# Performance work log

Hardware: AMD Instinct MI355X
Metric: run time of the kernel (lower is better)

Reference implementation:

```python
import jax, jax.numpy as jnp
import numpy as np

DIM = 128
H = 8
HD = DIM // H
NL = 6
DFF = 2048
EPS = 1e-5
S2S_STEPS = 6


def _ln(x, g, b):
    m = jnp.mean(x, -1, keepdims=True)
    v = jnp.mean(jnp.square(x - m), -1, keepdims=True)
    return (x - m) / jnp.sqrt(v + EPS) * g + b


def _lstm_step(x, h, c, wih, whh, bih, bhh):
    # torch LSTM gate order: i, f, g, o
    gates = x @ wih.T + bih + h @ whh.T + bhh
    i, f, g, o = jnp.split(gates, 4, axis=-1)
    c = jax.nn.sigmoid(f) * c + jax.nn.sigmoid(i) * jnp.tanh(g)
    h = jax.nn.sigmoid(o) * jnp.tanh(c)
    return h, c


def setup_inputs() -> dict:
    key = jax.random.key(0)
    ks = iter(jax.random.split(key, 16))
    n = lambda shape: jax.random.normal(next(ks), shape, jnp.float32) * 0.02
    inp = {
        "data": jax.random.normal(next(ks), (64, 256, 3), jnp.float32),
        "lin0_w": n((DIM, 3)), "lin0_b": jnp.zeros((DIM,), jnp.float32),
        "attn_in_w": n((NL, 3 * DIM, DIM)), "attn_in_b": jnp.zeros((NL, 3 * DIM), jnp.float32),
        "attn_out_w": n((NL, DIM, DIM)), "attn_out_b": jnp.zeros((NL, DIM), jnp.float32),
        "ln1_g": jnp.ones((NL, DIM), jnp.float32), "ln1_b": jnp.zeros((NL, DIM), jnp.float32),
        "ff_w1": n((NL, DFF, DIM)), "ff_b1": jnp.zeros((NL, DFF), jnp.float32),
        "ff_w2": n((NL, DIM, DFF)), "ff_b2": jnp.zeros((NL, DIM), jnp.float32),
        "ln2_g": jnp.ones((NL, DIM), jnp.float32), "ln2_b": jnp.zeros((NL, DIM), jnp.float32),
        "s2s_wih": n((4 * DIM, 2 * DIM)), "s2s_whh": n((4 * DIM, DIM)),
        "s2s_bih": jnp.zeros((4 * DIM,), jnp.float32), "s2s_bhh": jnp.zeros((4 * DIM,), jnp.float32),
        "mem_wih": n((4 * DIM, 2 * DIM)), "mem_whh": n((4 * DIM, DIM)),
        "mem_bih": jnp.zeros((4 * DIM,), jnp.float32), "mem_bhh": jnp.zeros((4 * DIM,), jnp.float32),
        "lin1_w": n((DIM, DIM)), "lin1_b": jnp.zeros((DIM,), jnp.float32),
        "lin3_w": n((1, DIM)), "lin3_b": jnp.zeros((1,), jnp.float32),
    }
    return inp


def reference(data, lin0_w, lin0_b, attn_in_w, attn_in_b, attn_out_w, attn_out_b,
              ln1_g, ln1_b, ff_w1, ff_b1, ff_w2, ff_b2, ln2_g, ln2_b,
              s2s_wih, s2s_whh, s2s_bih, s2s_bhh,
              mem_wih, mem_whh, mem_bih, mem_bhh,
              lin1_w, lin1_b, lin3_w, lin3_b):
    x = jax.nn.relu(data @ lin0_w.T + lin0_b)  # [S=64, B=256, D]
    S, B, _ = x.shape
    # torch TransformerEncoder with batch_first=False: attention over axis 0,
    # axis 1 is the transformer batch. Post-norm layers (norm_first=False), relu FFN.
    for l in range(NL):
        qkv = x @ attn_in_w[l].T + attn_in_b[l]
        q, k, v = jnp.split(qkv, 3, axis=-1)
        q = q.reshape(S, B, H, HD)
        k = k.reshape(S, B, H, HD)
        v = v.reshape(S, B, H, HD)
        scores = jnp.einsum('sbhd,tbhd->bhst', q, k) / np.float32(np.sqrt(HD))
        attn = jax.nn.softmax(scores, axis=-1)
        ao = jnp.einsum('bhst,tbhd->sbhd', attn, v).reshape(S, B, DIM)
        x = _ln(x + ao @ attn_out_w[l].T + attn_out_b[l], ln1_g[l], ln1_b[l])
        ff = jax.nn.relu(x @ ff_w1[l].T + ff_b1[l]) @ ff_w2[l].T + ff_b2[l]
        x = _ln(x + ff, ln2_g[l], ln2_b[l])
    # Set2Set pooling: bidxs assign segment = axis-0 index for each block of
    # num_atoms consecutive rows of flatten(out,0,1), i.e. pool over axis 1.
    q_star = jnp.zeros((S, 2 * DIM), x.dtype)
    h = jnp.zeros((S, DIM), x.dtype)
    c = jnp.zeros((S, DIM), x.dtype)
    for _ in range(S2S_STEPS):
        h, c = _lstm_step(q_star, h, c, s2s_wih, s2s_whh, s2s_bih, s2s_bhh)
        e = jnp.einsum('bnd,bd->bn', x, h)          # [S, num_atoms]
        a = jax.nn.softmax(e, axis=-1)              # segment softmax (uniform segs)
        r = jnp.einsum('bn,bnd->bd', a, x)          # segment weighted sum
        q_star = jnp.concatenate([h, r], axis=-1)   # [S, 2D]
    # memory LSTM: seq_len 1, zero initial state (states=None branch)
    hx = jnp.zeros((S, DIM), x.dtype)
    cx = jnp.zeros((S, DIM), x.dtype)
    hx, cx = _lstm_step(q_star, hx, cx, mem_wih, mem_whh, mem_bih, mem_bhh)
    o = jax.nn.relu(hx @ lin1_w.T + lin1_b)
    v_out = (o @ lin3_w.T + lin3_b)[None]  # [1, S, 1]
    return v_out, hx[None], cx[None]
```

## Files before the change

kernel.cpp:

```cpp
#include <hip/hip_runtime.h>
#include <math.h>


typedef _Float16 __attribute__((ext_vector_type(8))) f16x8;
typedef __attribute__((ext_vector_type(4))) float f32x4;
typedef _Float16 __attribute__((ext_vector_type(2))) h16x2;

__device__ __forceinline__ unsigned short f2h(float f) {
  union { _Float16 h; unsigned short s; } x; x.h = (_Float16)f; return x.s;
}
__device__ __forceinline__ float h2f(unsigned short u) {
  union { unsigned short s; _Float16 h; } x; x.s = u; return (float)x.h;
}
__device__ __forceinline__ unsigned packh(float a, float b) {
  return (unsigned)f2h(a) | ((unsigned)f2h(b) << 16);
}
__device__ __forceinline__ float hlo(unsigned u) {
  union { unsigned short s; _Float16 h; } x; x.s = (unsigned short)(u & 0xffff);
  return (float)x.h;
}
__device__ __forceinline__ float hhi(unsigned u) {
  union { unsigned short s; _Float16 h; } x; x.s = (unsigned short)(u >> 16);
  return (float)x.h;
}
__device__ __forceinline__ float fdot2u(unsigned a, unsigned b, float c) {
#if __has_builtin(__builtin_amdgcn_fdot2)
  union U { unsigned u; h16x2 h; };
  U x, y; x.u = a; y.u = b;
  return __builtin_amdgcn_fdot2(x.h, y.h, c, false);
#else
  return c + hlo(a) * hlo(b) + hhi(a) * hhi(b);
#endif
}
__device__ __forceinline__ float sigf(float x) { return 1.f / (1.f + expf(-x)); }

__device__ __forceinline__ void gl2lds16(const void* g, void* l) {
  __builtin_amdgcn_global_load_lds(
      (const __attribute__((address_space(1))) unsigned int*)g,
      (__attribute__((address_space(3))) unsigned int*)l, 16, 0, 0);
}

__global__ __launch_bounds__(256) void convw_kernel(
    const float* __restrict__ aiw, const float* __restrict__ aow,
    const float* __restrict__ w1, const float* __restrict__ w2,
    const float* __restrict__ wih, const float* __restrict__ whh,
    const float* __restrict__ mwih,
    unsigned short* __restrict__ o0, unsigned short* __restrict__ o1,
    unsigned short* __restrict__ o2, unsigned short* __restrict__ o3,
    unsigned short* __restrict__ o4, unsigned short* __restrict__ o5,
    unsigned short* __restrict__ o6) {
  int i = blockIdx.x * 256 + threadIdx.x;
  if (i < 294912) {
    int l = i / 49152, o = i % 49152;
    int j = o & 7, fr = (o >> 3) & 15, fq = (o >> 7) & 3, ks = (o >> 9) & 3,
        rb = o >> 11;
    o0[i] = f2h(aiw[l * 49152 + (rb * 16 + fr) * 128 + ks * 32 + fq * 8 + j]);
  } else if (i < 393216) {
    int ii = i - 294912;
    int l = ii / 16384, o = ii % 16384;
    int j = o & 7, fr = (o >> 3) & 15, fq = (o >> 7) & 3, ks = (o >> 9) & 3,
        rb = o >> 11;
    o1[ii] = f2h(aow[l * 16384 + (rb * 16 + fr) * 128 + ks * 32 + fq * 8 + j]);
  } else if (i < 1966080) {
    int ii = i - 393216;
    int l = ii >> 18, o = ii & 262143;
    int j = o & 7, fr = (o >> 3) & 15, fq = (o >> 7) & 3, ks = (o >> 9) & 3,
        rb = o >> 11;
    o2[ii] = f2h(w1[l * 262144 + (rb * 16 + fr) * 128 + ks * 32 + fq * 8 + j]);
  } else if (i < 3538944) {
    int ii = i - 1966080;
    int l = ii >> 18, o = ii & 262143;
    int j = o & 7, fr = (o >> 3) & 15, fq = (o >> 7) & 3, ks = (o >> 9) & 63,
        rb = o >> 15;
    o3[ii] = f2h(w2[l * 262144 + (rb * 16 + fr) * 2048 + ks * 32 + fq * 8 + j]);
  } else if (i < 3670016) {
    int j = i - 3538944; o4[j] = f2h(wih[j]);
  } else if (i < 3735552) {
    int j = i - 3670016; o5[j] = f2h(whh[j]);
  } else {
    int j = i - 3735552; o6[j] = f2h(mwih[j]);
  }
}

__global__ __launch_bounds__(256) void lin0_kernel(
    const float* __restrict__ data, const float* __restrict__ w,
    const float* __restrict__ b, float* __restrict__ x,
    unsigned short* __restrict__ xb) {
  int i = blockIdx.x * 256 + threadIdx.x;
  int n = i >> 7, d = i & 127;
  float v = b[d] + data[n * 3 + 0] * w[d * 3 + 0]
                 + data[n * 3 + 1] * w[d * 3 + 1]
                 + data[n * 3 + 2] * w[d * 3 + 2];
  v = fmaxf(v, 0.0f);
  x[i] = v;
  xb[i] = f2h(v);
}

__global__ __launch_bounds__(512) void layer_kernel(
    const unsigned short* __restrict__ xbg,
    const unsigned short* __restrict__ wqkv, const float* __restrict__ bqkv,
    const unsigned short* __restrict__ wout, const float* __restrict__ bout,
    const float* __restrict__ ln1g, const float* __restrict__ ln1b,
    const unsigned short* __restrict__ w1, const float* __restrict__ b1,
    const unsigned short* __restrict__ w2, const float* __restrict__ b2,
    const float* __restrict__ ln2g, const float* __restrict__ ln2b,
    float* __restrict__ xio, unsigned short* __restrict__ xbo) {
  __shared__ __align__(16) unsigned short Xs[64 * 128];
  __shared__ __align__(16) unsigned short Ws[256 * 128];
  __shared__ __align__(16) unsigned short U1[128 * 128];
  __shared__ __align__(16) unsigned short U2[128 * 128];
  __shared__ __align__(16) uint4 zchunk;
  __shared__ float psum[8][64], psq[8][64];
  __shared__ float2 stats[64];

  unsigned short* Qs = U1;
  unsigned short* Ks2 = U1 + 8192;
  unsigned short* VT = U2;
  unsigned short* AOs = U2 + 8192;

  int tid = threadIdx.x, w = tid >> 6, lane = tid & 63;
  int b = blockIdx.x;
  int r4 = lane >> 4, cs = lane & 15;
  int fr = lane & 15, fq = lane >> 4;

  if (tid == 0) zchunk = make_uint4(0u, 0u, 0u, 0u);

#pragma unroll
  for (int i = 0; i < 2; i++) {
    int issue = w * 2 + i;
    int row = issue * 4 + r4;
    int g = cs ^ (row & 7);
    gl2lds16(xbg + (size_t)(row * 256 + b) * 128 + g * 8,
             (char*)Xs + issue * 1024);
  }
  f16x8 bqk[4][2];
#pragma unroll
  for (int ks = 0; ks < 4; ks++)
#pragma unroll
    for (int ni = 0; ni < 2; ni++)
      bqk[ks][ni] = *(const f16x8*)(wqkv + (w * 2 + ni) * 2048 + ks * 512 +
                                    fq * 128 + fr * 8);
  __syncthreads();

  f16x8 xfragA[4][4];
#pragma unroll
  for (int ks = 0; ks < 4; ks++)
#pragma unroll
    for (int mi = 0; mi < 4; mi++) {
      int row = mi * 16 + fr;
      int kq = (ks * 4 + fq) ^ (row & 7);
      xfragA[ks][mi] = *(const f16x8*)(Xs + row * 128 + kq * 8);
    }

  {
    f32x4 acc[4][2];
#pragma unroll
    for (int i = 0; i < 4; i++)
#pragma unroll
      for (int j = 0; j < 2; j++) acc[i][j] = (f32x4){0.f, 0.f, 0.f, 0.f};
#pragma unroll
    for (int ks = 0; ks < 4; ks++)
#pragma unroll
      for (int mi = 0; mi < 4; mi++)
#pragma unroll
        for (int ni = 0; ni < 2; ni++)
          acc[mi][ni] = __builtin_amdgcn_mfma_f32_16x16x32_f16(
              xfragA[ks][mi], bqk[ks][ni], acc[mi][ni], 0, 0, 0);
#pragma unroll
    for (int ni = 0; ni < 2; ni++) {
      int c = (w * 2 + ni) * 16 + fr;
      float bv = bqkv[c];
      unsigned short* dst = (c < 128) ? Qs : Ks2;
      int cc = c & 127;
#pragma unroll
      for (int mi = 0; mi < 4; mi++)
#pragma unroll
        for (int r = 0; r < 4; r++) {
          int row = mi * 16 + fq * 4 + r;
          dst[row * 128 + (((cc >> 3) ^ (row & 7)) << 3) + (cc & 7)] =
              f2h(acc[mi][ni][r] + bv);
        }
    }
  }
  f16x8 bv4[4];
#pragma unroll
  for (int ks = 0; ks < 4; ks++)
    bv4[ks] = *(const f16x8*)(wqkv + (16 + w) * 2048 + ks * 512 + fq * 128 +
                              fr * 8);
  __syncthreads();

  {
    f32x4 acc[4];
#pragma unroll
    for (int i = 0; i < 4; i++) acc[i] = (f32x4){0.f, 0.f, 0.f, 0.f};
#pragma unroll
    for (int ks = 0; ks < 4; ks++)
#pragma unroll
      for (int mi = 0; mi < 4; mi++)
        acc[mi] = __builtin_amdgcn_mfma_f32_16x16x32_f16(xfragA[ks][mi],
                                                         bv4[ks], acc[mi],
                                                         0, 0, 0);
    int f = w * 16 + fr;
    float bv = bqkv[256 + f];
#pragma unroll
    for (int mi = 0; mi < 4; mi++)
#pragma unroll
      for (int r = 0; r < 4; r++) {
        int srow = mi * 16 + fq * 4 + r;
        VT[f * 64 + (((srow >> 3) ^ (f & 7)) << 3) + (srow & 7)] =
            f2h(acc[mi][r] + bv);
      }
  }
  __syncthreads();

  {
    int h = w;
    unsigned short* Pb = Ws + w * 4096;
    f32x4 sc[4][4];
#pragma unroll
    for (int i = 0; i < 4; i++)
#pragma unroll
      for (int j = 0; j < 4; j++) sc[i][j] = (f32x4){0.f, 0.f, 0.f, 0.f};
    {
      f16x8 af[4], bf[4];
#pragma unroll
      for (int mi = 0; mi < 4; mi++) {
        int row = mi * 16 + fr;
        const unsigned short* pa =
            (fq < 2) ? (Qs + row * 128 + (((h * 2 + fq) ^ (row & 7)) << 3))
                     : (const unsigned short*)&zchunk;
        af[mi] = *(const f16x8*)pa;
      }
#pragma unroll
      for (int ti = 0; ti < 4; ti++) {
        int trow = ti * 16 + fr;
        const unsigned short* pb =
            (fq < 2) ? (Ks2 + trow * 128 + (((h * 2 + fq) ^ (trow & 7)) << 3))
                     : (const unsigned short*)&zchunk;
        bf[ti] = *(const f16x8*)pb;
      }
#pragma unroll
      for (int mi = 0; mi < 4; mi++)
#pragma unroll
        for (int ti = 0; ti < 4; ti++)
          sc[mi][ti] = __builtin_amdgcn_mfma_f32_16x16x32_f16(
              af[mi], bf[ti], sc[mi][ti], 0, 0, 0);
    }
#pragma unroll
    for (int mi = 0; mi < 4; mi++) {
#pragma unroll
      for (int r = 0; r < 4; r++) {
        float m = -1e30f;
#pragma unroll
        for (int ti = 0; ti < 4; ti++) m = fmaxf(m, sc[mi][ti][r]);
        m = fmaxf(m, __shfl_xor(m, 1, 64));
        m = fmaxf(m, __shfl_xor(m, 2, 64));
        m = fmaxf(m, __shfl_xor(m, 4, 64));
        m = fmaxf(m, __shfl_xor(m, 8, 64));
        m *= 0.25f;
        float ss = 0.f;
#pragma unroll
        for (int ti = 0; ti < 4; ti++) {
          float p = expf(sc[mi][ti][r] * 0.25f - m);
          sc[mi][ti][r] = p;
          ss += p;
        }
        ss += __shfl_xor(ss, 1, 64);
        ss += __shfl_xor(ss, 2, 64);
        ss += __shfl_xor(ss, 4, 64);
        ss += __shfl_xor(ss, 8, 64);
        float inv = 1.f / ss;
        int prow = mi * 16 + fq * 4 + r;
#pragma unroll
        for (int ti = 0; ti < 4; ti++) {
          int t = ti * 16 + fr;
          Pb[prow * 64 + (((t >> 3) ^ (prow & 7)) << 3) + (t & 7)] =
              f2h(sc[mi][ti][r] * inv);
        }
      }
    }
    f32x4 po[4];
#pragma unroll
    for (int i = 0; i < 4; i++) po[i] = (f32x4){0.f, 0.f, 0.f, 0.f};
#pragma unroll
    for (int ks2 = 0; ks2 < 2; ks2++) {
      f16x8 af[4], bf;
#pragma unroll
      for (int si = 0; si < 4; si++) {
        int prow = si * 16 + fr;
        int kq = (ks2 * 4 + fq) ^ (prow & 7);
        af[si] = *(const f16x8*)(Pb + prow * 64 + kq * 8);
      }
      {
        int vrow = h * 16 + fr;
        int kq = (ks2 * 4 + fq) ^ (vrow & 7);
        bf = *(const f16x8*)(VT + vrow * 64 + kq * 8);
      }
#pragma unroll
      for (int si = 0; si < 4; si++)
        po[si] = __builtin_amdgcn_mfma_f32_16x16x32_f16(af[si], bf, po[si],
                                                        0, 0, 0);
    }
#pragma unroll
    for (int si = 0; si < 4; si++)
#pragma unroll
      for (int r = 0; r < 4; r++) {
        int arow = si * 16 + fq * 4 + r;
        int c = h * 16 + fr;
        AOs[arow * 128 + (((c >> 3) ^ (arow & 7)) << 3) + (c & 7)] =
            f2h(po[si][r]);
      }
  }
  f16x8 bwo[4];
#pragma unroll
  for (int ks = 0; ks < 4; ks++)
    bwo[ks] = *(const f16x8*)(wout + w * 2048 + ks * 512 + fq * 128 + fr * 8);
  __syncthreads();

  {
    f32x4 acc[4];
#pragma unroll
    for (int i = 0; i < 4; i++) acc[i] = (f32x4){0.f, 0.f, 0.f, 0.f};
#pragma unroll
    for (int ks = 0; ks < 4; ks++) {
      f16x8 af[4];
#pragma unroll
      for (int si = 0; si < 4; si++) {
        int row = si * 16 + fr;
        int kq = (ks * 4 + fq) ^ (row & 7);
        af[si] = *(const f16x8*)(AOs + row * 128 + kq * 8);
      }
#pragma unroll
      for (int si = 0; si < 4; si++)
        acc[si] = __builtin_amdgcn_mfma_f32_16x16x32_f16(af[si], bwo[ks],
                                                         acc[si], 0, 0, 0);
    }
    int c = w * 16 + fr;
    float bv = bout[c];
    float vv4[4][4];
    float sums[4][4], sqs[4][4];
#pragma unroll
    for (int si = 0; si < 4; si++)
#pragma unroll
      for (int r = 0; r < 4; r++) {
        int row = si * 16 + fq * 4 + r;
        float v = acc[si][r] + bv + xio[(size_t)(row * 256 + b) * 128 + c];
        vv4[si][r] = v;
        sums[si][r] = v;
        sqs[si][r] = v * v;
      }
#pragma unroll
    for (int d = 1; d < 16; d <<= 1) {
#pragma unroll
      for (int si = 0; si < 4; si++)
#pragma unroll
        for (int r = 0; r < 4; r++) {
          sums[si][r] += __shfl_xor(sums[si][r], d, 64);
          sqs[si][r] += __shfl_xor(sqs[si][r], d, 64);
        }
    }
    if (fr == 0) {
#pragma unroll
      for (int si = 0; si < 4; si++)
#pragma unroll
        for (int r = 0; r < 4; r++) {
          int row = si * 16 + fq * 4 + r;
          psum[w][row] = sums[si][r];
          psq[w][row] = sqs[si][r];
        }
    }
    __syncthreads();
    if (tid < 64) {
      float S = 0.f, Q = 0.f;
#pragma unroll
      for (int ww = 0; ww < 8; ww++) { S += psum[ww][tid]; Q += psq[ww][tid]; }
      float m = S * (1.f / 128.f);
      float var = Q * (1.f / 128.f) - m * m;
      stats[tid] = make_float2(m, rsqrtf(var + 1e-5f));
    }
    __syncthreads();
    float gl = ln1g[c], bl = ln1b[c];
#pragma unroll
    for (int si = 0; si < 4; si++)
#pragma unroll
      for (int r = 0; r < 4; r++) {
        int row = si * 16 + fq * 4 + r;
        float2 st2 = stats[row];
        float y = (vv4[si][r] - st2.x) * st2.y * gl + bl;
        Xs[row * 128 + (((c >> 3) ^ (row & 7)) << 3) + (c & 7)] = f2h(y);
      }
  }
  __syncthreads();

  f16x8 xfragF[4][4];
#pragma unroll
  for (int ks = 0; ks < 4; ks++)
#pragma unroll
    for (int mi = 0; mi < 4; mi++) {
      int row = mi * 16 + fr;
      int kq = (ks * 4 + fq) ^ (row & 7);
      xfragF[ks][mi] = *(const f16x8*)(Xs + row * 128 + kq * 8);
    }

  f32x4 acc2[4];
#pragma unroll
  for (int i = 0; i < 4; i++) acc2[i] = (f32x4){0.f, 0.f, 0.f, 0.f};

  for (int c = 0; c < 16; c++) {
    unsigned short* Hcur = Ws + (c & 1) * 8192;
    f16x8 bw1[4], bw2[4];
#pragma unroll
    for (int ks = 0; ks < 4; ks++)
      bw1[ks] = *(const f16x8*)(w1 + (size_t)(c * 8 + w) * 2048 + ks * 512 +
                                fq * 128 + fr * 8);
#pragma unroll
    for (int ks = 0; ks < 4; ks++)
      bw2[ks] = *(const f16x8*)(w2 + (size_t)w * 32768 + (c * 4 + ks) * 512 +
                                fq * 128 + fr * 8);
    f32x4 acc1[4];
#pragma unroll
    for (int i = 0; i < 4; i++) acc1[i] = (f32x4){0.f, 0.f, 0.f, 0.f};
#pragma unroll
    for (int ks = 0; ks < 4; ks++)
#pragma unroll
      for (int mi = 0; mi < 4; mi++)
        acc1[mi] = __builtin_amdgcn_mfma_f32_16x16x32_f16(xfragF[ks][mi],
                                                          bw1[ks], acc1[mi],
                                                          0, 0, 0);
    {
      int col = w * 16 + fr;
      float bv = b1[c * 128 + col];
#pragma unroll
      for (int mi = 0; mi < 4; mi++)
#pragma unroll
        for (int r = 0; r < 4; r++) {
          int row = mi * 16 + fq * 4 + r;
          Hcur[row * 128 + (((col >> 3) ^ (row & 7)) << 3) + (col & 7)] =
              f2h(fmaxf(acc1[mi][r] + bv, 0.f));
        }
    }
    __syncthreads();
#pragma unroll
    for (int ks = 0; ks < 4; ks++) {
      f16x8 af[4];
#pragma unroll
      for (int si = 0; si < 4; si++) {
        int row = si * 16 + fr;
        int kq = (ks * 4 + fq) ^ (row & 7);
        af[si] = *(const f16x8*)(Hcur + row * 128 + kq * 8);
      }
#pragma unroll
      for (int si = 0; si < 4; si++)
        acc2[si] = __builtin_amdgcn_mfma_f32_16x16x32_f16(af[si], bw2[ks],
                                                          acc2[si], 0, 0, 0);
    }
  }

  {
    int c = w * 16 + fr;
    float bv = b2[c];
    float vv4[4][4];
    float sums[4][4], sqs[4][4];
#pragma unroll
    for (int si = 0; si < 4; si++)
#pragma unroll
      for (int r = 0; r < 4; r++) {
        int row = si * 16 + fq * 4 + r;
        float resid =
            h2f(Xs[row * 128 + (((c >> 3) ^ (row & 7)) << 3) + (c & 7)]);
        float v = acc2[si][r] + bv + resid;
        vv4[si][r] = v;
        sums[si][r] = v;
        sqs[si][r] = v * v;
      }
#pragma unroll
    for (int d = 1; d < 16; d <<= 1) {
#pragma unroll
      for (int si = 0; si < 4; si++)
#pragma unroll
        for (int r = 0; r < 4; r++) {
          sums[si][r] += __shfl_xor(sums[si][r], d, 64);
          sqs[si][r] += __shfl_xor(sqs[si][r], d, 64);
        }
    }
    if (fr == 0) {
#pragma unroll
      for (int si = 0; si < 4; si++)
#pragma unroll
        for (int r = 0; r < 4; r++) {
          int row = si * 16 + fq * 4 + r;
          psum[w][row] = sums[si][r];
          psq[w][row] = sqs[si][r];
        }
    }
    __syncthreads();
    if (tid < 64) {
      float S = 0.f, Q = 0.f;
#pragma unroll
      for (int ww = 0; ww < 8; ww++) { S += psum[ww][tid]; Q += psq[ww][tid]; }
      float m = S * (1.f / 128.f);
      float var = Q * (1.f / 128.f) - m * m;
      stats[tid] = make_float2(m, rsqrtf(var + 1e-5f));
    }
    __syncthreads();
    float gl = ln2g[c], bl = ln2b[c];
#pragma unroll
    for (int si = 0; si < 4; si++)
#pragma unroll
      for (int r = 0; r < 4; r++) {
        int row = si * 16 + fq * 4 + r;
        float2 st = stats[row];
        float y = (vv4[si][r] - st.x) * st.y * gl + bl;
        size_t o = (size_t)(row * 256 + b) * 128 + c;
        xio[o] = y;
        xbo[o] = f2h(y);
      }
  }
}

__global__ __launch_bounds__(512, 1) void s2s_kernel(
    const unsigned short* __restrict__ xb,
    const unsigned short* __restrict__ wihh,
    const unsigned short* __restrict__ whhh,
    const float* __restrict__ bih, const float* __restrict__ bhh,
    const unsigned short* __restrict__ mwihh,
    const float* __restrict__ mbih, const float* __restrict__ mbhh,
    const float* __restrict__ l1w, const float* __restrict__ l1b,
    const float* __restrict__ l3w, const float* __restrict__ l3b,
    float* __restrict__ out) {
  __shared__ __align__(16) unsigned xl[256 * 65];
  __shared__ __align__(16) unsigned qu[128];
  __shared__ __align__(16) float cst[128];
  __shared__ __align__(16) float gates[512];
  __shared__ __align__(16) float red[256];
  __shared__ __align__(16) float aw[256];
  int s = blockIdx.x, t = threadIdx.x, lane = t & 63, w = t >> 6;

  uint4 wreg[32], ureg[16];
  {
    const uint4* wp = (const uint4*)(wihh + (size_t)t * 256);
#pragma unroll
    for (int i = 0; i < 32; i++) wreg[i] = wp[i];
    const uint4* up = (const uint4*)(whhh + (size_t)t * 128);
#pragma unroll
    for (int i = 0; i < 16; i++) ureg[i] = up[i];
  }

  const uint4* xs4 = (const uint4*)(xb + (size_t)s * 32768);
#pragma unroll
  for (int it = 0; it < 8; it++) {
    int f = it * 512 + t;
    uint4 v = xs4[f];
    int n = f >> 4, jc = (f & 15) * 4;
    unsigned* dst = xl + n * 65 + jc;
    dst[0] = v.x; dst[1] = v.y; dst[2] = v.z; dst[3] = v.w;
  }
  if (t < 128) cst[t] = 0.f;
  __syncthreads();

  const uint4* q4 = (const uint4*)qu;
  float bsum = bih[t] + bhh[t];

  for (int step = 0; step < 6; step++) {
    if (step > 0) {
      float a0 = 0.f, a1 = 0.f, a2 = 0.f, a3 = 0.f;
#pragma unroll
      for (int i = 0; i < 16; i++) {
        uint4 qv = q4[i];
        a0 = fdot2u(wreg[i].x, qv.x, a0);
        a1 = fdot2u(wreg[i].y, qv.y, a1);
        a2 = fdot2u(wreg[i].z, qv.z, a2);
        a3 = fdot2u(wreg[i].w, qv.w, a3);
        a0 = fdot2u(ureg[i].x, qv.x, a0);
        a1 = fdot2u(ureg[i].y, qv.y, a1);
        a2 = fdot2u(ureg[i].z, qv.z, a2);
        a3 = fdot2u(ureg[i].w, qv.w, a3);
      }
#pragma unroll
      for (int i = 16; i < 32; i++) {
        uint4 qv = q4[i];
        a0 = fdot2u(wreg[i].x, qv.x, a0);
        a1 = fdot2u(wreg[i].y, qv.y, a1);
        a2 = fdot2u(wreg[i].z, qv.z, a2);
        a3 = fdot2u(wreg[i].w, qv.w, a3);
      }
      gates[t] = bsum + ((a0 + a1) + (a2 + a3));
    } else {
      gates[t] = bsum;
    }
    __syncthreads();
    if (t < 128) {
      float ig = sigf(gates[t]), fg = sigf(gates[128 + t]);
      float gg = tanhf(gates[256 + t]), og = sigf(gates[384 + t]);
      float cn = fg * cst[t] + ig * gg;
      cst[t] = cn;
      float hn = og * tanhf(cn);
      float hp = __shfl_xor(hn, 1, 64);
      if ((t & 1) == 0) qu[t >> 1] = packh(hn, hp);
    }
    __syncthreads();
    if (step > 0) {
      int n = t >> 1, p = t & 1;
      const unsigned* xr = xl + n * 65 + p * 32;
      float e0 = 0.f, e1 = 0.f;
#pragma unroll 8
      for (int i = 0; i < 32; i += 2) {
        e0 = fdot2u(xr[i], qu[p * 32 + i], e0);
        e1 = fdot2u(xr[i + 1], qu[p * 32 + i + 1], e1);
      }
      float e = e0 + e1;
      e += __shfl_xor(e, 1, 64);
      if (p == 0) red[n] = e;
      __syncthreads();
      float v0 = red[lane], v1 = red[64 + lane];
      float v2 = red[128 + lane], v3 = red[192 + lane];
      float m = fmaxf(fmaxf(v0, v1), fmaxf(v2, v3));
#pragma unroll
      for (int d = 1; d < 64; d <<= 1) m = fmaxf(m, __shfl_xor(m, d, 64));
      float p0 = expf(v0 - m), p1 = expf(v1 - m);
      float p2 = expf(v2 - m), p3 = expf(v3 - m);
      float ss = p0 + p1 + p2 + p3;
#pragma unroll
      for (int d = 1; d < 64; d <<= 1) ss += __shfl_xor(ss, d, 64);
      float Sinv = 1.f / ss;
      if (w == 0) {
        aw[lane] = p0 * Sinv; aw[64 + lane] = p1 * Sinv;
        aw[128 + lane] = p2 * Sinv; aw[192 + lane] = p3 * Sinv;
      }
    } else {
      if (t < 256) aw[t] = 1.f / 256.f;
    }
    __syncthreads();
    {
      int d = t & 127, grp = t >> 7;
      const unsigned* xc = xl + grp * 64 * 65 + (d >> 1);
      int hi = d & 1;
      const float* ap = aw + grp * 64;
      float r = 0.f;
#pragma unroll 8
      for (int n2 = 0; n2 < 64; n2++) {
        unsigned u = xc[n2 * 65];
        r += ap[n2] * (hi ? hhi(u) : hlo(u));
      }
      gates[t] = r;
    }
    __syncthreads();
    if (t < 128) {
      float rd = gates[t] + gates[128 + t] + gates[256 + t] + gates[384 + t];
      float rp = __shfl_xor(rd, 1, 64);
      if ((t & 1) == 0) qu[64 + (t >> 1)] = packh(rd, rp);
    }
    __syncthreads();
  }
  {
    float a0 = 0.f, a1 = 0.f, a2 = 0.f, a3 = 0.f;
    const uint4* mp = (const uint4*)(mwihh + (size_t)t * 256);
#pragma unroll 8
    for (int i = 0; i < 32; i++) {
      uint4 wv = mp[i], qv = q4[i];
      a0 = fdot2u(wv.x, qv.x, a0);
      a1 = fdot2u(wv.y, qv.y, a1);
      a2 = fdot2u(wv.z, qv.z, a2);
      a3 = fdot2u(wv.w, qv.w, a3);
    }
    gates[t] = mbih[t] + mbhh[t] + ((a0 + a1) + (a2 + a3));
  }
  __syncthreads();
  if (t < 128) {
    float ig = sigf(gates[t]);
    float gg = tanhf(gates[256 + t]);
    float og = sigf(gates[384 + t]);
    float cx = ig * gg;
    float hx = og * tanhf(cx);
    cst[t] = hx;
    out[64 + s * 128 + t] = hx;
    out[64 + 8192 + s * 128 + t] = cx;
  }
  __syncthreads();
  if (t < 128) {
    float acc = l1b[t];
    const float4* w4 = (const float4*)(l1w + (size_t)t * 128);
    const float4* h4 = (const float4*)cst;
#pragma unroll 8
    for (int k = 0; k < 32; k++) {
      float4 a = w4[k], b = h4[k];
      acc += a.x * b.x + a.y * b.y + a.z * b.z + a.w * b.w;
    }
    red[t] = fmaxf(acc, 0.f) * l3w[t];
  } else if (t < 256) {
    red[t] = 0.f;
  }
  __syncthreads();
  for (int off = 128; off; off >>= 1) {
    if (t < off) red[t] += red[t + off];
    __syncthreads();
  }
  if (t == 0) out[s] = red[0] + l3b[0];
}

extern "C" void kernel_launch(void* const* d_in, const int* in_sizes, int n_in,
                              void* d_out, int out_size, void* d_ws,
                              size_t ws_size, hipStream_t stream) {
  const float* data       = (const float*)d_in[0];
  const float* lin0_w     = (const float*)d_in[1];
  const float* lin0_b     = (const float*)d_in[2];
  const float* attn_in_w  = (const float*)d_in[3];
  const float* attn_in_b  = (const float*)d_in[4];
  const float* attn_out_w = (const float*)d_in[5];
  const float* attn_out_b = (const float*)d_in[6];
  const float* ln1_g      = (const float*)d_in[7];
  const float* ln1_b      = (const float*)d_in[8];
  const float* ff_w1      = (const float*)d_in[9];
  const float* ff_b1      = (const float*)d_in[10];
  const float* ff_w2      = (const float*)d_in[11];
  const float* ff_b2      = (const float*)d_in[12];
  const float* ln2_g      = (const float*)d_in[13];
  const float* ln2_b      = (const float*)d_in[14];
  const float* s2s_wih    = (const float*)d_in[15];
  const float* s2s_whh    = (const float*)d_in[16];
  const float* s2s_bih    = (const float*)d_in[17];
  const float* s2s_bhh    = (const float*)d_in[18];
  const float* mem_wih    = (const float*)d_in[19];
  const float* mem_bih    = (const float*)d_in[21];
  const float* mem_bhh    = (const float*)d_in[22];
  const float* lin1_w     = (const float*)d_in[23];
  const float* lin1_b     = (const float*)d_in[24];
  const float* lin3_w     = (const float*)d_in[25];
  const float* lin3_b     = (const float*)d_in[26];
  float* out = (float*)d_out;

  char* p = (char*)d_ws;
  float* x = (float*)p;                      p += (size_t)16384 * 128 * 4;
  unsigned short* xb = (unsigned short*)p;   p += (size_t)16384 * 128 * 2;
  unsigned short* wqkv = (unsigned short*)p; p += (size_t)294912 * 2;
  unsigned short* wout = (unsigned short*)p; p += (size_t)98304 * 2;
  unsigned short* w1h = (unsigned short*)p;  p += (size_t)1572864 * 2;
  unsigned short* w2h = (unsigned short*)p;  p += (size_t)1572864 * 2;
  unsigned short* wihh = (unsigned short*)p; p += (size_t)131072 * 2;
  unsigned short* whhh = (unsigned short*)p; p += (size_t)65536 * 2;
  unsigned short* mwihh = (unsigned short*)p; p += (size_t)131072 * 2;

  convw_kernel<<<15104, 256, 0, stream>>>(
      attn_in_w, attn_out_w, ff_w1, ff_w2, s2s_wih, s2s_whh, mem_wih,
      wqkv, wout, w1h, w2h, wihh, whhh, mwihh);
  lin0_kernel<<<8192, 256, 0, stream>>>(data, lin0_w, lin0_b, x, xb);

  for (int l = 0; l < 6; l++) {
    layer_kernel<<<256, 512, 0, stream>>>(
        xb, wqkv + (size_t)l * 49152, attn_in_b + l * 384,
        wout + (size_t)l * 16384, attn_out_b + l * 128,
        ln1_g + l * 128, ln1_b + l * 128,
        w1h + (size_t)l * 262144, ff_b1 + l * 2048,
        w2h + (size_t)l * 262144, ff_b2 + l * 128,
        ln2_g + l * 128, ln2_b + l * 128, x, xb);
  }

  s2s_kernel<<<64, 512, 0, stream>>>(
      xb, wihh, whhh, s2s_bih, s2s_bhh,
      mwihh, mem_bih, mem_bhh, lin1_w, lin1_b, lin3_w, lin3_b, out);
}
```

Measured before the change: 459.4 us.

## Split layer kernel into two blocks per batch column with half-row ownership

The fused transformer layer kernel now launches 512 blocks of 256 threads instead of 256 blocks of 512. Each block still computes full Q/K/V for all 64 sequence rows, but handles attention output, the out-projection, LayerNorms and the FFN for only its half (32 rows). Shared memory is trimmed by reusing buffers (Q/K region for P and FFN hidden, Xs for attention output), which lets two blocks fit per CU. This doubles the grid on a 256-CU device to improve occupancy and latency hiding, at the cost of duplicating the QKV projection in both blocks and reloading weight fragments inside loops instead of keeping them in registers.

```diff
diff --git a/kernel.cpp b/kernel.cpp
--- a/kernel.cpp
+++ b/kernel.cpp
@@ -96,7 +96,7 @@
   xb[i] = f2h(v);
 }
 
-__global__ __launch_bounds__(512) void layer_kernel(
+__global__ __launch_bounds__(256, 2) void layer_kernel(
     const unsigned short* __restrict__ xbg,
     const unsigned short* __restrict__ wqkv, const float* __restrict__ bqkv,
     const unsigned short* __restrict__ wout, const float* __restrict__ bout,
@@ -106,40 +106,30 @@
     const float* __restrict__ ln2g, const float* __restrict__ ln2b,
     float* __restrict__ xio, unsigned short* __restrict__ xbo) {
   __shared__ __align__(16) unsigned short Xs[64 * 128];
-  __shared__ __align__(16) unsigned short Ws[256 * 128];
-  __shared__ __align__(16) unsigned short U1[128 * 128];
-  __shared__ __align__(16) unsigned short U2[128 * 128];
+  __shared__ __align__(16) unsigned short QKP[16384];
+  __shared__ __align__(16) unsigned short VT[128 * 64];
   __shared__ __align__(16) uint4 zchunk;
-  __shared__ float psum[8][64], psq[8][64];
-  __shared__ float2 stats[64];
-
-  unsigned short* Qs = U1;
-  unsigned short* Ks2 = U1 + 8192;
-  unsigned short* VT = U2;
-  unsigned short* AOs = U2 + 8192;
+  __shared__ float psum[4][32], psq[4][32];
+  __shared__ float2 stats[32];
+
+  unsigned short* Qs = QKP;
+  unsigned short* Ks2 = QKP + 8192;
 
   int tid = threadIdx.x, w = tid >> 6, lane = tid & 63;
-  int b = blockIdx.x;
+  int b = blockIdx.x >> 1, half = blockIdx.x & 1;
   int r4 = lane >> 4, cs = lane & 15;
   int fr = lane & 15, fq = lane >> 4;
 
   if (tid == 0) zchunk = make_uint4(0u, 0u, 0u, 0u);
 
 #pragma unroll
-  for (int i = 0; i < 2; i++) {
-    int issue = w * 2 + i;
+  for (int i = 0; i < 4; i++) {
+    int issue = w * 4 + i;
     int row = issue * 4 + r4;
     int g = cs ^ (row & 7);
     gl2lds16(xbg + (size_t)(row * 256 + b) * 128 + g * 8,
              (char*)Xs + issue * 1024);
   }
-  f16x8 bqk[4][2];
-#pragma unroll
-  for (int ks = 0; ks < 4; ks++)
-#pragma unroll
-    for (int ni = 0; ni < 2; ni++)
-      bqk[ks][ni] = *(const f16x8*)(wqkv + (w * 2 + ni) * 2048 + ks * 512 +
-                                    fq * 128 + fr * 8);
   __syncthreads();
 
   f16x8 xfragA[4][4];
@@ -153,22 +143,28 @@
     }
 
   {
-    f32x4 acc[4][2];
+    f32x4 acc[4][4];
 #pragma unroll
     for (int i = 0; i < 4; i++)
 #pragma unroll
-      for (int j = 0; j < 2; j++) acc[i][j] = (f32x4){0.f, 0.f, 0.f, 0.f};
-#pragma unroll
-    for (int ks = 0; ks < 4; ks++)
+      for (int j = 0; j < 4; j++) acc[i][j] = (f32x4){0.f, 0.f, 0.f, 0.f};
+#pragma unroll
+    for (int ks = 0; ks < 4; ks++) {
+      f16x8 bf[4];
+#pragma unroll
+      for (int ni = 0; ni < 4; ni++)
+        bf[ni] = *(const f16x8*)(wqkv + (w * 4 + ni) * 2048 + ks * 512 +
+                                 fq * 128 + fr * 8);
 #pragma unroll
       for (int mi = 0; mi < 4; mi++)
 #pragma unroll
-        for (int ni = 0; ni < 2; ni++)
+        for (int ni = 0; ni < 4; ni++)
           acc[mi][ni] = __builtin_amdgcn_mfma_f32_16x16x32_f16(
-              xfragA[ks][mi], bqk[ks][ni], acc[mi][ni], 0, 0, 0);
-#pragma unroll
-    for (int ni = 0; ni < 2; ni++) {
-      int c = (w * 2 + ni) * 16 + fr;
+              xfragA[ks][mi], bf[ni], acc[mi][ni], 0, 0, 0);
+    }
+#pragma unroll
+    for (int ni = 0; ni < 4; ni++) {
+      int c = (w * 4 + ni) * 16 + fr;
       float bv = bqkv[c];
       unsigned short* dst = (c < 128) ? Qs : Ks2;
       int cc = c & 127;
@@ -182,54 +178,56 @@
         }
     }
   }
-  f16x8 bv4[4];
-#pragma unroll
-  for (int ks = 0; ks < 4; ks++)
-    bv4[ks] = *(const f16x8*)(wqkv + (16 + w) * 2048 + ks * 512 + fq * 128 +
-                              fr * 8);
   __syncthreads();
 
   {
-    f32x4 acc[4];
-#pragma unroll
-    for (int i = 0; i < 4; i++) acc[i] = (f32x4){0.f, 0.f, 0.f, 0.f};
-#pragma unroll
-    for (int ks = 0; ks < 4; ks++)
+    f32x4 acc[2][4];
+#pragma unroll
+    for (int i = 0; i < 2; i++)
+#pragma unroll
+      for (int j = 0; j < 4; j++) acc[i][j] = (f32x4){0.f, 0.f, 0.f, 0.f};
+#pragma unroll
+    for (int ks = 0; ks < 4; ks++) {
+      f16x8 bf[2];
+#pragma unroll
+      for (int fi = 0; fi < 2; fi++)
+        bf[fi] = *(const f16x8*)(wqkv + (16 + w * 2 + fi) * 2048 + ks * 512 +
+                                 fq * 128 + fr * 8);
+#pragma unroll
+      for (int fi = 0; fi < 2; fi++)
+#pragma unroll
+        for (int mi = 0; mi < 4; mi++)
+          acc[fi][mi] = __builtin_amdgcn_mfma_f32_16x16x32_f16(
+              xfragA[ks][mi], bf[fi], acc[fi][mi], 0, 0, 0);
+    }
+#pragma unroll
+    for (int fi = 0; fi < 2; fi++) {
+      int f = (w * 2 + fi) * 16 + fr;
+      float bv = bqkv[256 + f];
 #pragma unroll
       for (int mi = 0; mi < 4; mi++)
-        acc[mi] = __builtin_amdgcn_mfma_f32_16x16x32_f16(xfragA[ks][mi],
-                                                         bv4[ks], acc[mi],
-                                                         0, 0, 0);
-    int f = w * 16 + fr;
-    float bv = bqkv[256 + f];
-#pragma unroll
-    for (int mi = 0; mi < 4; mi++)
-#pragma unroll
-      for (int r = 0; r < 4; r++) {
-        int srow = mi * 16 + fq * 4 + r;
-        VT[f * 64 + (((srow >> 3) ^ (f & 7)) << 3) + (srow & 7)] =
-            f2h(acc[mi][r] + bv);
-      }
+#pragma unroll
+        for (int r = 0; r < 4; r++) {
+          int srow = mi * 16 + fq * 4 + r;
+          VT[f * 64 + (((srow >> 3) ^ (f & 7)) << 3) + (srow & 7)] =
+              f2h(acc[fi][mi][r] + bv);
+        }
+    }
   }
   __syncthreads();
 
   {
-    int h = w;
-    unsigned short* Pb = Ws + w * 4096;
-    f32x4 sc[4][4];
-#pragma unroll
-    for (int i = 0; i < 4; i++)
-#pragma unroll
-      for (int j = 0; j < 4; j++) sc[i][j] = (f32x4){0.f, 0.f, 0.f, 0.f};
-    {
-      f16x8 af[4], bf[4];
-#pragma unroll
-      for (int mi = 0; mi < 4; mi++) {
-        int row = mi * 16 + fr;
+    f16x8 afH[2][2], bfH[2][4];
+#pragma unroll
+    for (int hi = 0; hi < 2; hi++) {
+      int h = w * 2 + hi;
+#pragma unroll
+      for (int mi2 = 0; mi2 < 2; mi2++) {
+        int rowg = half * 32 + mi2 * 16 + fr;
         const unsigned short* pa =
-            (fq < 2) ? (Qs + row * 128 + (((h * 2 + fq) ^ (row & 7)) << 3))
+            (fq < 2) ? (Qs + rowg * 128 + (((h * 2 + fq) ^ (rowg & 7)) << 3))
                      : (const unsigned short*)&zchunk;
-        af[mi] = *(const f16x8*)pa;
+        afH[hi][mi2] = *(const f16x8*)pa;
       }
 #pragma unroll
       for (int ti = 0; ti < 4; ti++) {
@@ -237,284 +235,332 @@
         const unsigned short* pb =
             (fq < 2) ? (Ks2 + trow * 128 + (((h * 2 + fq) ^ (trow & 7)) << 3))
                      : (const unsigned short*)&zchunk;
-        bf[ti] = *(const f16x8*)pb;
-      }
-#pragma unroll
-      for (int mi = 0; mi < 4; mi++)
+        bfH[hi][ti] = *(const f16x8*)pb;
+      }
+    }
+    __syncthreads();
+
+#pragma unroll
+    for (int hi = 0; hi < 2; hi++) {
+      int h = w * 2 + hi;
+      unsigned short* Pb = QKP + (w * 2 + hi) * 2048;
+      f32x4 sc[2][4];
+#pragma unroll
+      for (int i = 0; i < 2; i++)
+#pragma unroll
+        for (int j = 0; j < 4; j++) sc[i][j] = (f32x4){0.f, 0.f, 0.f, 0.f};
+#pragma unroll
+      for (int mi2 = 0; mi2 < 2; mi2++)
 #pragma unroll
         for (int ti = 0; ti < 4; ti++)
-          sc[mi][ti] = __builtin_amdgcn_mfma_f32_16x16x32_f16(
-              af[mi], bf[ti], sc[mi][ti], 0, 0, 0);
-    }
-#pragma unroll
-    for (int mi = 0; mi < 4; mi++) {
-#pragma unroll
-      for (int r = 0; r < 4; r++) {
-        float m = -1e30f;
-#pragma unroll
-        for (int ti = 0; ti < 4; ti++) m = fmaxf(m, sc[mi][ti][r]);
-        m = fmaxf(m, __shfl_xor(m, 1, 64));
-        m = fmaxf(m, __shfl_xor(m, 2, 64));
-        m = fmaxf(m, __shfl_xor(m, 4, 64));
-        m = fmaxf(m, __shfl_xor(m, 8, 64));
-        m *= 0.25f;
-        float ss = 0.f;
-#pragma unroll
-        for (int ti = 0; ti < 4; ti++) {
-          float p = expf(sc[mi][ti][r] * 0.25f - m);
-          sc[mi][ti][r] = p;
-          ss += p;
-        }
-        ss += __shfl_xor(ss, 1, 64);
-        ss += __shfl_xor(ss, 2, 64);
-        ss += __shfl_xor(ss, 4, 64);
-        ss += __shfl_xor(ss, 8, 64);
-        float inv = 1.f / ss;
-        int prow = mi * 16 + fq * 4 + r;
-#pragma unroll
-        for (int ti = 0; ti < 4; ti++) {
-          int t = ti * 16 + fr;
-          Pb[prow * 64 + (((t >> 3) ^ (prow & 7)) << 3) + (t & 7)] =
-              f2h(sc[mi][ti][r] * inv);
-        }
-      }
-    }
-    f32x4 po[4];
-#pragma unroll
-    for (int i = 0; i < 4; i++) po[i] = (f32x4){0.f, 0.f, 0.f, 0.f};
-#pragma unroll
-    for (int ks2 = 0; ks2 < 2; ks2++) {
-      f16x8 af[4], bf;
-#pragma unroll
-      for (int si = 0; si < 4; si++) {
-        int prow = si * 16 + fr;
-        int kq = (ks2 * 4 + fq) ^ (prow & 7);
-        af[si] = *(const f16x8*)(Pb + prow * 64 + kq * 8);
-      }
-      {
-        int vrow = h * 16 + fr;
-        int kq = (ks2 * 4 + fq) ^ (vrow & 7);
-        bf = *(const f16x8*)(VT + vrow * 64 + kq * 8);
-      }
-#pragma unroll
-      for (int si = 0; si < 4; si++)
-        po[si] = __builtin_amdgcn_mfma_f32_16x16x32_f16(af[si], bf, po[si],
-                                                        0, 0, 0);
-    }
-#pragma unroll
-    for (int si = 0; si < 4; si++)
-#pragma unroll
-      for (int r = 0; r < 4; r++) {
-        int arow = si * 16 + fq * 4 + r;
-        int c = h * 16 + fr;
-        AOs[arow * 128 + (((c >> 3) ^ (arow & 7)) << 3) + (c & 7)] =
-            f2h(po[si][r]);
-      }
-  }
-  f16x8 bwo[4];
-#pragma unroll
-  for (int ks = 0; ks < 4; ks++)
-    bwo[ks] = *(const f16x8*)(wout + w * 2048 + ks * 512 + fq * 128 + fr * 8);
+          sc[mi2][ti] = __builtin_amdgcn_mfma_f32_16x16x32_f16(
+              afH[hi][mi2], bfH[hi][ti], sc[mi2][ti], 0, 0, 0);
+#pragma unroll
+      for (int mi2 = 0; mi2 < 2; mi2++) {
+#pragma unroll
+        for (int r = 0; r < 4; r++) {
+          float m = -1e30f;
+#pragma unroll
+          for (int ti = 0; ti < 4; ti++) m = fmaxf(m, sc[mi2][ti][r]);
+          m = fmaxf(m, __shfl_xor(m, 1, 64));
+          m = fmaxf(m, __shfl_xor(m, 2, 64));
+          m = fmaxf(m, __shfl_xor(m, 4, 64));
+          m = fmaxf(m, __shfl_xor(m, 8, 64));
+          m *= 0.25f;
+          float ss = 0.f;
+#pragma unroll
+          for (int ti = 0; ti < 4; ti++) {
+            float p = expf(sc[mi2][ti][r] * 0.25f - m);
+            sc[mi2][ti][r] = p;
+            ss += p;
+          }
+          ss += __shfl_xor(ss, 1, 64);
+          ss += __shfl_xor(ss, 2, 64);
+          ss += __shfl_xor(ss, 4, 64);
+          ss += __shfl_xor(ss, 8, 64);
+          float inv = 1.f / ss;
+          int prow = mi2 * 16 + fq * 4 + r;
+#pragma unroll
+          for (int ti = 0; ti < 4; ti++) {
+            int t = ti * 16 + fr;
+            Pb[prow * 64 + (((t >> 3) ^ (prow & 7)) << 3) + (t & 7)] =
+                f2h(sc[mi2][ti][r] * inv);
+          }
+        }
+      }
+      f32x4 po[2];
+#pragma unroll
+      for (int i = 0; i < 2; i++) po[i] = (f32x4){0.f, 0.f, 0.f, 0.f};
+#pragma unroll
+      for (int ks2 = 0; ks2 < 2; ks2++) {
+        f16x8 af[2], bf;
+#pragma unroll
+        for (int si2 = 0; si2 < 2; si2++) {
+          int prow = si2 * 16 + fr;
+          int kq = (ks2 * 4 + fq) ^ (prow & 7);
+          af[si2] = *(const f16x8*)(Pb + prow * 64 + kq * 8);
+        }
+        {
+          int vrow = h * 16 + fr;
+          int kq = (ks2 * 4 + fq) ^ (vrow & 7);
+          bf = *(const f16x8*)(VT + vrow * 64 + kq * 8);
+        }
+#pragma unroll
+        for (int si2 = 0; si2 < 2; si2++)
+          po[si2] = __builtin_amdgcn_mfma_f32_16x16x32_f16(af[si2], bf,
+                                                           po[si2], 0, 0, 0);
+      }
+#pragma unroll
+      for (int si2 = 0; si2 < 2; si2++)
+#pragma unroll
+        for (int r = 0; r < 4; r++) {
+          int arow = si2 * 16 + fq * 4 + r;
+          int c = h * 16 + fr;
+          Xs[arow * 128 + (((c >> 3) ^ (arow & 7)) << 3) + (c & 7)] =
+              f2h(po[si2][r]);
+        }
+    }
+  }
   __syncthreads();
 
+  float vv4[2][2][4];
   {
-    f32x4 acc[4];
-#pragma unroll
-    for (int i = 0; i < 4; i++) acc[i] = (f32x4){0.f, 0.f, 0.f, 0.f};
+    f32x4 acc[2][2];
+#pragma unroll
+    for (int i = 0; i < 2; i++)
+#pragma unroll
+      for (int j = 0; j < 2; j++) acc[i][j] = (f32x4){0.f, 0.f, 0.f, 0.f};
 #pragma unroll
     for (int ks = 0; ks < 4; ks++) {
-      f16x8 af[4];
-#pragma unroll
-      for (int si = 0; si < 4; si++) {
-        int row = si * 16 + fr;
-        int kq = (ks * 4 + fq) ^ (row & 7);
-        af[si] = *(const f16x8*)(AOs + row * 128 + kq * 8);
-      }
-#pragma unroll
-      for (int si = 0; si < 4; si++)
-        acc[si] = __builtin_amdgcn_mfma_f32_16x16x32_f16(af[si], bwo[ks],
-                                                         acc[si], 0, 0, 0);
-    }
-    int c = w * 16 + fr;
-    float bv = bout[c];
-    float vv4[4][4];
-    float sums[4][4], sqs[4][4];
-#pragma unroll
-    for (int si = 0; si < 4; si++)
-#pragma unroll
-      for (int r = 0; r < 4; r++) {
-        int row = si * 16 + fq * 4 + r;
-        float v = acc[si][r] + bv + xio[(size_t)(row * 256 + b) * 128 + c];
-        vv4[si][r] = v;
-        sums[si][r] = v;
-        sqs[si][r] = v * v;
-      }
+      f16x8 af[2], bwo[2];
+#pragma unroll
+      for (int si2 = 0; si2 < 2; si2++) {
+        int rowl = si2 * 16 + fr;
+        int kq = (ks * 4 + fq) ^ (rowl & 7);
+        af[si2] = *(const f16x8*)(Xs + rowl * 128 + kq * 8);
+      }
+#pragma unroll
+      for (int ni = 0; ni < 2; ni++)
+        bwo[ni] = *(const f16x8*)(wout + (w * 2 + ni) * 2048 + ks * 512 +
+                                  fq * 128 + fr * 8);
+#pragma unroll
+      for (int si2 = 0; si2 < 2; si2++)
+#pragma unroll
+        for (int ni = 0; ni < 2; ni++)
+          acc[si2][ni] = __builtin_amdgcn_mfma_f32_16x16x32_f16(
+              af[si2], bwo[ni], acc[si2][ni], 0, 0, 0);
+    }
+    float sums[2][4], sqs[2][4];
+#pragma unroll
+    for (int si2 = 0; si2 < 2; si2++)
+#pragma unroll
+      for (int r = 0; r < 4; r++) { sums[si2][r] = 0.f; sqs[si2][r] = 0.f; }
+#pragma unroll
+    for (int ni = 0; ni < 2; ni++) {
+      int c = (w * 2 + ni) * 16 + fr;
+      float bv = bout[c];
+#pragma unroll
+      for (int si2 = 0; si2 < 2; si2++)
+#pragma unroll
+        for (int r = 0; r < 4; r++) {
+          int rowl = si2 * 16 + fq * 4 + r;
+          int rowg = half * 32 + rowl;
+          float v = acc[si2][ni][r] + bv + xio[(size_t)(rowg * 256 + b) * 128 + c];
+          vv4[ni][si2][r] = v;
+          sums[si2][r] += v;
+          sqs[si2][r] += v * v;
+        }
+    }
 #pragma unroll
     for (int d = 1; d < 16; d <<= 1) {
 #pragma unroll
-      for (int si = 0; si < 4; si++)
-#pragma unroll
-        for (int r = 0; r < 4; r++) {
-          sums[si][r] += __shfl_xor(sums[si][r], d, 64);
-          sqs[si][r] += __shfl_xor(sqs[si][r], d, 64);
+      for (int si2 = 0; si2 < 2; si2++)
+#pragma unroll
+        for (int r = 0; r < 4; r++) {
+          sums[si2][r] += __shfl_xor(sums[si2][r], d, 64);
+          sqs[si2][r] += __shfl_xor(sqs[si2][r], d, 64);
         }
     }
     if (fr == 0) {
 #pragma unroll
-      for (int si = 0; si < 4; si++)
-#pragma unroll
-        for (int r = 0; r < 4; r++) {
-          int row = si * 16 + fq * 4 + r;
-          psum[w][row] = sums[si][r];
-          psq[w][row] = sqs[si][r];
-        }
-    }
-    __syncthreads();
-    if (tid < 64) {
+      for (int si2 = 0; si2 < 2; si2++)
+#pragma unroll
+        for (int r = 0; r < 4; r++) {
+          int rowl = si2 * 16 + fq * 4 + r;
+          psum[w][rowl] = sums[si2][r];
+          psq[w][rowl] = sqs[si2][r];
+        }
+    }
+    __syncthreads();
+    if (tid < 32) {
       float S = 0.f, Q = 0.f;
 #pragma unroll
-      for (int ww = 0; ww < 8; ww++) { S += psum[ww][tid]; Q += psq[ww][tid]; }
+      for (int ww = 0; ww < 4; ww++) { S += psum[ww][tid]; Q += psq[ww][tid]; }
       float m = S * (1.f / 128.f);
       float var = Q * (1.f / 128.f) - m * m;
       stats[tid] = make_float2(m, rsqrtf(var + 1e-5f));
     }
     __syncthreads();
-    float gl = ln1g[c], bl = ln1b[c];
-#pragma unroll
-    for (int si = 0; si < 4; si++)
-#pragma unroll
-      for (int r = 0; r < 4; r++) {
-        int row = si * 16 + fq * 4 + r;
-        float2 st2 = stats[row];
-        float y = (vv4[si][r] - st2.x) * st2.y * gl + bl;
-        Xs[row * 128 + (((c >> 3) ^ (row & 7)) << 3) + (c & 7)] = f2h(y);
-      }
+#pragma unroll
+    for (int ni = 0; ni < 2; ni++) {
+      int c = (w * 2 + ni) * 16 + fr;
+      float gl = ln1g[c], bl = ln1b[c];
+#pragma unroll
+      for (int si2 = 0; si2 < 2; si2++)
+#pragma unroll
+        for (int r = 0; r < 4; r++) {
+          int rowl = si2 * 16 + fq * 4 + r;
+          float2 st2 = stats[rowl];
+          float y = (vv4[ni][si2][r] - st2.x) * st2.y * gl + bl;
+          Xs[rowl * 128 + (((c >> 3) ^ (rowl & 7)) << 3) + (c & 7)] = f2h(y);
+        }
+    }
   }
   __syncthreads();
 
-  f16x8 xfragF[4][4];
+  f16x8 xfragF[4][2];
 #pragma unroll
   for (int ks = 0; ks < 4; ks++)
 #pragma unroll
-    for (int mi = 0; mi < 4; mi++) {
-      int row = mi * 16 + fr;
-      int kq = (ks * 4 + fq) ^ (row & 7);
-      xfragF[ks][mi] = *(const f16x8*)(Xs + row * 128 + kq * 8);
-    }
-
-  f32x4 acc2[4];
-#pragma unroll
-  for (int i = 0; i < 4; i++) acc2[i] = (f32x4){0.f, 0.f, 0.f, 0.f};
+    for (int mi2 = 0; mi2 < 2; mi2++) {
+      int rowl = mi2 * 16 + fr;
+      int kq = (ks * 4 + fq) ^ (rowl & 7);
+      xfragF[ks][mi2] = *(const f16x8*)(Xs + rowl * 128 + kq * 8);
+    }
+
+  f32x4 acc2[2][2];
+#pragma unroll
+  for (int i = 0; i < 2; i++)
+#pragma unroll
+    for (int j = 0; j < 2; j++) acc2[i][j] = (f32x4){0.f, 0.f, 0.f, 0.f};
 
   for (int c = 0; c < 16; c++) {
-    unsigned short* Hcur = Ws + (c & 1) * 8192;
-    f16x8 bw1[4], bw2[4];
-#pragma unroll
-    for (int ks = 0; ks < 4; ks++)
-      bw1[ks] = *(const f16x8*)(w1 + (size_t)(c * 8 + w) * 2048 + ks * 512 +
-                                fq * 128 + fr * 8);
-#pragma unroll
-    for (int ks = 0; ks < 4; ks++)
-      bw2[ks] = *(const f16x8*)(w2 + (size_t)w * 32768 + (c * 4 + ks) * 512 +
-                                fq * 128 + fr * 8);
-    f32x4 acc1[4];
-#pragma unroll
-    for (int i = 0; i < 4; i++) acc1[i] = (f32x4){0.f, 0.f, 0.f, 0.f};
-#pragma unroll
-    for (int ks = 0; ks < 4; ks++)
-#pragma unroll
-      for (int mi = 0; mi < 4; mi++)
-        acc1[mi] = __builtin_amdgcn_mfma_f32_16x16x32_f16(xfragF[ks][mi],
-                                                          bw1[ks], acc1[mi],
-                                                          0, 0, 0);
-    {
-      int col = w * 16 + fr;
+    unsigned short* Hcur = QKP + (c & 1) * 4096;
+    f32x4 acc1[2][2];
+#pragma unroll
+    for (int i = 0; i < 2; i++)
+#pragma unroll
+      for (int j = 0; j < 2; j++) acc1[i][j] = (f32x4){0.f, 0.f, 0.f, 0.f};
+#pragma unroll
+    for (int ks = 0; ks < 4; ks++) {
+      f16x8 b1f[2];
+#pragma unroll
+      for (int ni = 0; ni < 2; ni++)
+        b1f[ni] = *(const f16x8*)(w1 + (size_t)(c * 8 + w * 2 + ni) * 2048 +
+                                  ks * 512 + fq * 128 + fr * 8);
+#pragma unroll
+      for (int mi2 = 0; mi2 < 2; mi2++)
+#pragma unroll
+        for (int ni = 0; ni < 2; ni++)
+          acc1[mi2][ni] = __builtin_amdgcn_mfma_f32_16x16x32_f16(
+              xfragF[ks][mi2], b1f[ni], acc1[mi2][ni], 0, 0, 0);
+    }
+#pragma unroll
+    for (int ni = 0; ni < 2; ni++) {
+      int col = (w * 2 + ni) * 16 + fr;
       float bv = b1[c * 128 + col];
 #pragma unroll
-      for (int mi = 0; mi < 4; mi++)
-#pragma unroll
-        for (int r = 0; r < 4; r++) {
-          int row = mi * 16 + fq * 4 + r;
-          Hcur[row * 128 + (((col >> 3) ^ (row & 7)) << 3) + (col & 7)] =
-              f2h(fmaxf(acc1[mi][r] + bv, 0.f));
+      for (int mi2 = 0; mi2 < 2; mi2++)
+#pragma unroll
+        for (int r = 0; r < 4; r++) {
+          int rowl = mi2 * 16 + fq * 4 + r;
+          Hcur[rowl * 128 + (((col >> 3) ^ (rowl & 7)) << 3) + (col & 7)] =
+              f2h(fmaxf(acc1[mi2][ni][r] + bv, 0.f));
         }
     }
     __syncthreads();
 #pragma unroll
     for (int ks = 0; ks < 4; ks++) {
-      f16x8 af[4];
-#pragma unroll
-      for (int si = 0; si < 4; si++) {
-        int row = si * 16 + fr;
-        int kq = (ks * 4 + fq) ^ (row & 7);
-        af[si] = *(const f16x8*)(Hcur + row * 128 + kq * 8);
-      }
-#pragma unroll
-      for (int si = 0; si < 4; si++)
-        acc2[si] = __builtin_amdgcn_mfma_f32_16x16x32_f16(af[si], bw2[ks],
-                                                          acc2[si], 0, 0, 0);
+      f16x8 af[2], b2f[2];
+#pragma unroll
+      for (int si2 = 0; si2 < 2; si2++) {
+        int rowl = si2 * 16 + fr;
+        int kq = (ks * 4 + fq) ^ (rowl & 7);
+        af[si2] = *(const f16x8*)(Hcur + rowl * 128 + kq * 8);
+      }
+#pragma unroll
+      for (int ni = 0; ni < 2; ni++)
+        b2f[ni] = *(const f16x8*)(w2 + (size_t)(w * 2 + ni) * 32768 +
+                                  (c * 4 + ks) * 512 + fq * 128 + fr * 8);
+#pragma unroll
+      for (int si2 = 0; si2 < 2; si2++)
+#pragma unroll
+        for (int ni = 0; ni < 2; ni++)
+          acc2[si2][ni] = __builtin_amdgcn_mfma_f32_16x16x32_f16(
+              af[si2], b2f[ni], acc2[si2][ni], 0, 0, 0);
     }
   }
 
   {
-    int c = w * 16 + fr;
-    float bv = b2[c];
-    float vv4[4][4];
-    float sums[4][4], sqs[4][4];
-#pragma unroll
-    for (int si = 0; si < 4; si++)
-#pragma unroll
-      for (int r = 0; r < 4; r++) {
-        int row = si * 16 + fq * 4 + r;
-        float resid =
-            h2f(Xs[row * 128 + (((c >> 3) ^ (row & 7)) << 3) + (c & 7)]);
-        float v = acc2[si][r] + bv + resid;
-        vv4[si][r] = v;
-        sums[si][r] = v;
-        sqs[si][r] = v * v;
-      }
+    float vvo[2][2][4];
+    float sums[2][4], sqs[2][4];
+#pragma unroll
+    for (int si2 = 0; si2 < 2; si2++)
+#pragma unroll
+      for (int r = 0; r < 4; r++) { sums[si2][r] = 0.f; sqs[si2][r] = 0.f; }
+#pragma unroll
+    for (int ni = 0; ni < 2; ni++) {
+      int c = (w * 2 + ni) * 16 + fr;
+      float bv = b2[c];
+#pragma unroll
+      for (int si2 = 0; si2 < 2; si2++)
+#pragma unroll
+        for (int r = 0; r < 4; r++) {
+          int rowl = si2 * 16 + fq * 4 + r;
+          float resid =
+              h2f(Xs[rowl * 128 + (((c >> 3) ^ (rowl & 7)) << 3) + (c & 7)]);
+          float v = acc2[si2][ni][r] + bv + resid;
+          vvo[ni][si2][r] = v;
+          sums[si2][r] += v;
+          sqs[si2][r] += v * v;
+        }
+    }
 #pragma unroll
     for (int d = 1; d < 16; d <<= 1) {
 #pragma unroll
-      for (int si = 0; si < 4; si++)
-#pragma unroll
-        for (int r = 0; r < 4; r++) {
-          sums[si][r] += __shfl_xor(sums[si][r], d, 64);
-          sqs[si][r] += __shfl_xor(sqs[si][r], d, 64);
+      for (int si2 = 0; si2 < 2; si2++)
+#pragma unroll
+        for (int r = 0; r < 4; r++) {
+          sums[si2][r] += __shfl_xor(sums[si2][r], d, 64);
+          sqs[si2][r] += __shfl_xor(sqs[si2][r], d, 64);
         }
     }
     if (fr == 0) {
 #pragma unroll
-      for (int si = 0; si < 4; si++)
-#pragma unroll
-        for (int r = 0; r < 4; r++) {
-          int row = si * 16 + fq * 4 + r;
-          psum[w][row] = sums[si][r];
-          psq[w][row] = sqs[si][r];
-        }
-    }
-    __syncthreads();
-    if (tid < 64) {
+      for (int si2 = 0; si2 < 2; si2++)
+#pragma unroll
+        for (int r = 0; r < 4; r++) {
+          int rowl = si2 * 16 + fq * 4 + r;
+          psum[w][rowl] = sums[si2][r];
+          psq[w][rowl] = sqs[si2][r];
+        }
+    }
+    __syncthreads();
+    if (tid < 32) {
       float S = 0.f, Q = 0.f;
 #pragma unroll
-      for (int ww = 0; ww < 8; ww++) { S += psum[ww][tid]; Q += psq[ww][tid]; }
+      for (int ww = 0; ww < 4; ww++) { S += psum[ww][tid]; Q += psq[ww][tid]; }
       float m = S * (1.f / 128.f);
       float var = Q * (1.f / 128.f) - m * m;
       stats[tid] = make_float2(m, rsqrtf(var + 1e-5f));
     }
     __syncthreads();
-    float gl = ln2g[c], bl = ln2b[c];
-#pragma unroll
-    for (int si = 0; si < 4; si++)
-#pragma unroll
-      for (int r = 0; r < 4; r++) {
-        int row = si * 16 + fq * 4 + r;
-        float2 st = stats[row];
-        float y = (vv4[si][r] - st.x) * st.y * gl + bl;
-        size_t o = (size_t)(row * 256 + b) * 128 + c;
-        xio[o] = y;
-        xbo[o] = f2h(y);
-      }
+#pragma unroll
+    for (int ni = 0; ni < 2; ni++) {
+      int c = (w * 2 + ni) * 16 + fr;
+      float gl = ln2g[c], bl = ln2b[c];
+#pragma unroll
+      for (int si2 = 0; si2 < 2; si2++)
+#pragma unroll
+        for (int r = 0; r < 4; r++) {
+          int rowl = si2 * 16 + fq * 4 + r;
+          float2 st = stats[rowl];
+          float y = (vvo[ni][si2][r] - st.x) * st.y * gl + bl;
+          size_t o = (size_t)((half * 32 + rowl) * 256 + b) * 128 + c;
+          xio[o] = y;
+          xbo[o] = f2h(y);
+        }
+    }
   }
 }
 
@@ -746,7 +792,7 @@
   lin0_kernel<<<8192, 256, 0, stream>>>(data, lin0_w, lin0_b, x, xb);
 
   for (int l = 0; l < 6; l++) {
-    layer_kernel<<<256, 512, 0, stream>>>(
+    layer_kernel<<<512, 256, 0, stream>>>(
         xb, wqkv + (size_t)l * 49152, attn_in_b + l * 384,
         wout + (size_t)l * 16384, attn_out_b + l * 128,
         ln1_g + l * 128, ln1_b + l * 128,
```

After: 461.5 us. No clear change (+0.5%).
